# Performance work log

Hardware: AMD Instinct MI355X
Metric: run time of the kernel (lower is better)

Reference implementation:

```python
import jax, jax.numpy as jnp
import numpy as np

N_SEG = 64        # number of graphs in batch
NEG_SLOPE = 0.2   # PyG GATConv leaky_relu slope


def seg_softmax(vals, seg, num_segments):
    # vals: [E, H]; softmax over entries sharing the same segment id
    m = jax.ops.segment_max(vals, seg, num_segments=num_segments)
    m = jnp.where(jnp.isfinite(m), m, 0.0)  # guard empty segments
    e = jnp.exp(vals - m[seg])
    s = jax.ops.segment_sum(e, seg, num_segments=num_segments)
    return e / (s[seg] + 1e-16)


def setup_inputs() -> dict:
    key = jax.random.key(0)
    ks = jax.random.split(key, 16)
    N, E, Fin, H, C1, C2 = 50000, 800000, 128, 4, 32, 128
    x = jax.random.normal(ks[0], (N, Fin), jnp.float32)
    edge_index = jax.random.randint(ks[1], (2, E), 0, N)
    batch = jnp.sort(jax.random.randint(ks[2], (N,), 0, N_SEG))
    sc = lambda fan: 1.0 / np.sqrt(fan)
    W_gat = jax.random.normal(ks[3], (Fin, H * C1), jnp.float32) * sc(Fin)
    att_src = jax.random.normal(ks[4], (H, C1), jnp.float32) * sc(C1)
    att_dst = jax.random.normal(ks[5], (H, C1), jnp.float32) * sc(C1)
    b_gat = jnp.zeros((H * C1,), jnp.float32)
    bn1_w = jax.random.uniform(ks[6], (H * C1,), jnp.float32, 0.5, 1.5)
    bn1_b = jax.random.normal(ks[7], (H * C1,), jnp.float32) * 0.1
    W_gcn = jax.random.normal(ks[8], (H * C1, C2), jnp.float32) * sc(H * C1)
    b_gcn = jnp.zeros((C2,), jnp.float32)
    bn2_w = jax.random.uniform(ks[9], (C2,), jnp.float32, 0.5, 1.5)
    bn2_b = jax.random.normal(ks[10], (C2,), jnp.float32) * 0.1
    W_gate = jax.random.normal(ks[11], (C2, 1), jnp.float32) * sc(C2)
    b_gate = jnp.zeros((1,), jnp.float32)
    W_fc = jax.random.normal(ks[12], (C2, 1), jnp.float32) * sc(C2)
    b_fc = jnp.zeros((1,), jnp.float32)
    return dict(x=x, edge_index=edge_index, batch=batch, W_gat=W_gat,
                att_src=att_src, att_dst=att_dst, b_gat=b_gat,
                bn1_w=bn1_w, bn1_b=bn1_b, W_gcn=W_gcn, b_gcn=b_gcn,
                bn2_w=bn2_w, bn2_b=bn2_b, W_gate=W_gate, b_gate=b_gate,
                W_fc=W_fc, b_fc=b_fc)


def reference(x, edge_index, batch, W_gat, att_src, att_dst, b_gat,
              bn1_w, bn1_b, W_gcn, b_gcn, bn2_w, bn2_b,
              W_gate, b_gate, W_fc, b_fc):
    N = x.shape[0]
    H, C1 = att_src.shape
    loops = jnp.arange(N)
    src = jnp.concatenate([edge_index[0], loops])  # message source j
    dst = jnp.concatenate([edge_index[1], loops])  # aggregation target i

    # ---- GATConv (heads=4, concat, add_self_loops) ----
    h = (x @ W_gat).reshape(N, H, C1)                       # [N,H,C1]
    a_src = jnp.einsum('nhc,hc->nh', h, att_src)
    a_dst = jnp.einsum('nhc,hc->nh', h, att_dst)
    e = jax.nn.leaky_relu(a_src[src] + a_dst[dst], NEG_SLOPE)  # [E',H]
    alpha = seg_softmax(e, dst, N)
    msg = h[src] * alpha[..., None]                          # [E',H,C1]
    out1 = jax.ops.segment_sum(msg, dst, num_segments=N).reshape(N, H * C1) + b_gat
    out1 = jax.nn.elu(out1)
    out1 = out1 * bn1_w + bn1_b          # BatchNorm1d (eval: mean 0, var 1)
    # dropout: identity (eval mode)

    # ---- GCNConv (self-loops, symmetric normalization) ----
    deg = jax.ops.segment_sum(jnp.ones_like(dst, dtype=x.dtype), dst, num_segments=N)
    dinv = jax.lax.rsqrt(jnp.maximum(deg, 1.0))
    norm = dinv[src] * dinv[dst]                             # [E']
    h2 = out1 @ W_gcn                                        # [N,C2]
    out2 = jax.ops.segment_sum(h2[src] * norm[:, None], dst, num_segments=N) + b_gcn
    out2 = jax.nn.elu(out2)
    out2 = out2 * bn2_w + bn2_b

    # ---- GlobalAttention pooling ----
    gate = out2 @ W_gate + b_gate                            # [N,1]
    w = seg_softmax(gate, batch, N_SEG)
    graph_rep = jax.ops.segment_sum(w * out2, batch, num_segments=N_SEG)  # [G,C2]

    out = graph_rep @ W_fc + b_fc                            # [G,1]
    return out.squeeze(1)
```

## Files before the change

kernel.cpp:

```cpp
#include <hip/hip_runtime.h>
#include <math.h>


#define NEG_SLOPE 0.2f
#define BKT_BITS 7
#define BKT_SIZE 128
#define CHUNK_A 4096

typedef __attribute__((ext_vector_type(8))) short short8v;
typedef __attribute__((ext_vector_type(4))) float floatx4;

__device__ __forceinline__ int lower_bound_i(const int* a, int n, int key) {
    int lo = 0, hi = n;
    while (lo < hi) {
        int mid = (lo + hi) >> 1;
        if (a[mid] < key) lo = mid + 1; else hi = mid;
    }
    return lo;
}

__device__ __forceinline__ unsigned pack_bf16(float lo, float hi) {
    unsigned ua = __float_as_uint(lo);
    unsigned ub = __float_as_uint(hi);
    ua = ua + 0x7fffu + ((ua >> 16) & 1u);
    ub = ub + 0x7fffu + ((ub >> 16) & 1u);
    return (ua >> 16) | (ub & 0xffff0000u);
}

__device__ __forceinline__ unsigned short bf16_1(float v) {
    unsigned u = __float_as_uint(v);
    u = u + 0x7fffu + ((u >> 16) & 1u);
    return (unsigned short)(u >> 16);
}

__global__ __launch_bounds__(1024) void k_prep(
    const float* __restrict__ W1, const float* __restrict__ atts,
    const float* __restrict__ attd, const float* __restrict__ W2,
    unsigned short* __restrict__ Wt1, unsigned short* __restrict__ Wt2)
{
    if (blockIdx.x == 0) {
        for (int idx = threadIdx.x; idx < 144 * 128; idx += 1024) {
            int j = idx >> 7, i = idx & 127;
            float v;
            if (j < 128) v = W1[i * 128 + j];
            else if (j < 132) {
                int h = j - 128; float s = 0.f;
                for (int c = 0; c < 32; c++) s += W1[i * 128 + h * 32 + c] * atts[h * 32 + c];
                v = s;
            } else if (j < 136) {
                int h = j - 132; float s = 0.f;
                for (int c = 0; c < 32; c++) s += W1[i * 128 + h * 32 + c] * attd[h * 32 + c];
                v = s;
            } else v = 0.f;
            Wt1[idx] = bf16_1(v);
        }
    } else {
        for (int idx = threadIdx.x; idx < 144 * 128; idx += 1024) {
            int j = idx >> 7, i = idx & 127;
            Wt2[idx] = bf16_1(j < 128 ? W2[i * 128 + j] : 0.f);
        }
    }
}

__global__ __launch_bounds__(256) void k_gemm_mfma(
    const float* __restrict__ A, const unsigned short* __restrict__ Wt,
    unsigned* __restrict__ Cb, int N, int mode,
    const float* __restrict__ pb, const float* __restrict__ pw,
    const float* __restrict__ pb2, const float* __restrict__ dinv,
    float* __restrict__ aS, float* __restrict__ aD)
{
    __shared__ unsigned short sA[64 * 136];
    __shared__ unsigned short sB[144 * 136];
    const int tid = threadIdx.x;
    const int n0 = blockIdx.x * 64;

    {
        const uint4* Wg = (const uint4*)Wt;
#pragma unroll
        for (int i = 0; i < 9; i++) {
            int q = tid + 256 * i;
            uint4 v = Wg[q];
            int j = q >> 4, seg = q & 15;
            *(uint4*)(sB + j * 136 + seg * 8) = v;
        }
    }
    {
#pragma unroll
        for (int i = 0; i < 8; i++) {
            int g = tid + 256 * i;
            int r = g >> 5, w4 = g & 31;
            int gn = n0 + r;
            unsigned p0 = 0, p1 = 0;
            if (gn < N) {
                float4 v = *(const float4*)(A + (size_t)gn * 128 + w4 * 4);
                if (mode) {
                    int k = w4 * 4;
                    float4 bv = *(const float4*)(pb + k);
                    float4 wv = *(const float4*)(pw + k);
                    float4 b2 = *(const float4*)(pb2 + k);
                    float t;
                    t = v.x + bv.x; t = (t > 0.f) ? t : expm1f(t); v.x = t * wv.x + b2.x;
                    t = v.y + bv.y; t = (t > 0.f) ? t : expm1f(t); v.y = t * wv.y + b2.y;
                    t = v.z + bv.z; t = (t > 0.f) ? t : expm1f(t); v.z = t * wv.z + b2.z;
                    t = v.w + bv.w; t = (t > 0.f) ? t : expm1f(t); v.w = t * wv.w + b2.w;
                }
                p0 = pack_bf16(v.x, v.y);
                p1 = pack_bf16(v.z, v.w);
            }
            uint2 pv = make_uint2(p0, p1);
            *(uint2*)(sA + r * 136 + w4 * 4) = pv;
        }
    }
    __syncthreads();

    const int wid = tid >> 6, lane = tid & 63;
    const int quad = lane >> 4, l16 = lane & 15;

    floatx4 acc[9];
#pragma unroll
    for (int ct = 0; ct < 9; ct++) acc[ct] = (floatx4){0.f, 0.f, 0.f, 0.f};

    const unsigned short* pa = sA + (wid * 16 + l16) * 136 + quad * 8;
    const unsigned short* pbt = sB + l16 * 136 + quad * 8;
#pragma unroll
    for (int ks = 0; ks < 4; ks++) {
        short8v a = *(const short8v*)(pa + ks * 32);
#pragma unroll
        for (int ct = 0; ct < 9; ct++) {
            short8v b = *(const short8v*)(pbt + ct * (16 * 136) + ks * 32);
            acc[ct] = __builtin_amdgcn_mfma_f32_16x16x32_bf16(a, b, acc[ct], 0, 0, 0);
        }
    }

#pragma unroll
    for (int r = 0; r < 4; r++) {
        int n = n0 + wid * 16 + quad * 4 + r;
        if (n >= N) continue;
        float s = mode ? dinv[n] : 1.f;
#pragma unroll
        for (int ct = 0; ct < 4; ct++) {
            Cb[(size_t)n * 64 + ct * 16 + l16] =
                pack_bf16(acc[ct][r] * s, acc[ct + 4][r] * s);
        }
        if (mode == 0) {
            float e = acc[8][r];
            if (l16 < 4) aS[(size_t)n * 4 + l16] = e;
            else if (l16 < 8) aD[(size_t)n * 4 + (l16 - 4)] = e;
        }
    }
}

__global__ __launch_bounds__(256) void k_bhist(const int* __restrict__ dst,
                                               int* __restrict__ bcount,
                                               int E, int NB)
{
    __shared__ int h[512];
    const int tid = threadIdx.x;
    for (int i = tid; i < NB; i += 256) h[i] = 0;
    __syncthreads();
    int base = blockIdx.x * 2048;
#pragma unroll
    for (int k = 0; k < 8; k++) {
        int e = base + k * 256 + tid;
        if (e < E) atomicAdd(&h[dst[e] >> BKT_BITS], 1);
    }
    __syncthreads();
    for (int i = tid; i < NB; i += 256) {
        int c = h[i];
        if (c) atomicAdd(&bcount[i], c);
    }
}

__global__ __launch_bounds__(512) void k_bscan(const int* __restrict__ bcount,
                                               int* __restrict__ bb,
                                               int* __restrict__ bcur, int NB)
{
    __shared__ int sc[512];
    const int tid = threadIdx.x;
    int own = (tid < NB) ? bcount[tid] : 0;
    sc[tid] = own;
    __syncthreads();
    for (int st = 1; st < 512; st <<= 1) {
        int v = 0;
        if (tid >= st) v = sc[tid - st];
        __syncthreads();
        if (tid >= st) sc[tid] += v;
        __syncthreads();
    }
    int excl = sc[tid] - own;
    if (tid < NB) { bb[tid] = excl; bcur[tid] = excl; }
    if (tid == 511) { bb[NB] = sc[511]; bcur[NB] = sc[511]; }
}

__global__ __launch_bounds__(256) void k_binA(const int* __restrict__ ei,
                                              int* __restrict__ bcur,
                                              int2* __restrict__ pairs,
                                              int E, int NB)
{
    __shared__ int h[512];
    __shared__ int base[512];
    const int tid = threadIdx.x;
    for (int i = tid; i < NB + 1; i += 256) h[i] = 0;
    __syncthreads();
    const int c0 = blockIdx.x * CHUNK_A;
    int s[16], d[16], b[16];
#pragma unroll
    for (int k = 0; k < 16; k++) {
        int e = c0 + k * 256 + tid;
        bool v = e < E;
        s[k] = v ? ei[e] : 0;
        d[k] = v ? ei[E + e] : 0;
        b[k] = v ? (d[k] >> BKT_BITS) : NB;
        atomicAdd(&h[b[k]], 1);
    }
    __syncthreads();
    for (int i = tid; i < NB + 1; i += 256) {
        int c = h[i];
        base[i] = c ? atomicAdd(&bcur[i], c) : 0;
        h[i] = 0;
    }
    __syncthreads();
#pragma unroll
    for (int k = 0; k < 16; k++) {
        int r = atomicAdd(&h[b[k]], 1);
        pairs[base[b[k]] + r] = make_int2(s[k], d[k]);
    }
}

__global__ __launch_bounds__(256) void k_binB(const int2* __restrict__ pairs,
                                              const int* __restrict__ bb,
                                              int* __restrict__ csr,
                                              int* __restrict__ offs,
                                              float* __restrict__ dinv,
                                              int N, int NB, int E)
{
    __shared__ int hist[BKT_SIZE], start[BKT_SIZE], cur[BKT_SIZE];
    __shared__ int sc[BKT_SIZE];
    const int tid = threadIdx.x;
    const int b = blockIdx.x;
    const int d0 = b << BKT_BITS;
    const int pbg = bb[b], peg = bb[b + 1];

    if (tid < BKT_SIZE) { hist[tid] = 0; cur[tid] = 0; }
    __syncthreads();
    for (int i = pbg + tid; i < peg; i += 256)
        atomicAdd(&hist[pairs[i].y - d0], 1);
    __syncthreads();
    int own = (tid < BKT_SIZE) ? hist[tid] : 0;
    if (tid < BKT_SIZE) sc[tid] = own;
    __syncthreads();
    for (int st = 1; st < BKT_SIZE; st <<= 1) {
        int v = 0;
        bool act = (tid < BKT_SIZE) && (tid >= st);
        if (act) v = sc[tid - st];
        __syncthreads();
        if (act) sc[tid] += v;
        __syncthreads();
    }
    if (tid < BKT_SIZE) {
        int abs0 = pbg + (sc[tid] - own);
        start[tid] = abs0;
        int d = d0 + tid;
        if (d < N) {
            offs[d] = abs0;
            dinv[d] = rsqrtf((float)(own + 1));
        }
    }
    if (tid == 0 && b == NB - 1) offs[N] = E;
    __syncthreads();
    for (int i = pbg + tid; i < peg; i += 256) {
        int2 p = pairs[i];
        int ld = p.y - d0;
        int r = atomicAdd(&cur[ld], 1);
        csr[start[ld] + r] = p.x;
    }
}

__global__ __launch_bounds__(256) void k_gat_aggr(
    const unsigned* __restrict__ hb, const float* __restrict__ aSg,
    const float* __restrict__ aDg, const int* __restrict__ offs,
    const int* __restrict__ csr, float* __restrict__ raw1, int N)
{
    __shared__ __align__(16) float s_u[4][64][4];
    __shared__ int s_s[4][64];

    const int wid = threadIdx.x >> 6;
    const int lane = threadIdx.x & 63;
    const int n = blockIdx.x * 4 + wid;
    if (n >= N) return;

    const int beg = offs[n];
    const int cnt = offs[n + 1] - beg + 1;
    const float4 ad = *(const float4*)(aDg + (size_t)n * 4);
    const int hA = lane >> 5;
    const float* pu = &s_u[wid][0][2 * hA];
    const int* ps = &s_s[wid][0];

    float t0 = 0.f, t1 = 0.f, t2 = 0.f, t3 = 0.f;
    float accLo = 0.f, accHi = 0.f;

    for (int base = 0; base < cnt; base += 64) {
        int idx = base + lane;
        bool valid = idx < cnt;
        int src = n;
        if (valid && idx > 0) src = csr[beg + idx - 1];
        float u0 = 0.f, u1 = 0.f, u2 = 0.f, u3 = 0.f;
        if (valid) {
            float4 as = *(const float4*)(aSg + (size_t)src * 4);
            float l0 = as.x + ad.x; l0 = (l0 > 0.f) ? l0 : NEG_SLOPE * l0;
            float l1 = as.y + ad.y; l1 = (l1 > 0.f) ? l1 : NEG_SLOPE * l1;
            float l2 = as.z + ad.z; l2 = (l2 > 0.f) ? l2 : NEG_SLOPE * l2;
            float l3 = as.w + ad.w; l3 = (l3 > 0.f) ? l3 : NEG_SLOPE * l3;
            u0 = __expf(l0); u1 = __expf(l1); u2 = __expf(l2); u3 = __expf(l3);
        }
        t0 += u0; t1 += u1; t2 += u2; t3 += u3;
        s_s[wid][lane] = src;
        *(float4*)&s_u[wid][lane][0] = make_float4(u0, u2, u1, u3);

        int cc = min(64, cnt - base);
        int j = 0;
        for (; j + 8 <= cc; j += 8) {
            int sj[8]; float2 uj[8]; unsigned vv[8];
#pragma unroll
            for (int k = 0; k < 8; k++) sj[k] = ps[j + k];
#pragma unroll
            for (int k = 0; k < 8; k++) uj[k] = *(const float2*)&pu[(j + k) * 4];
#pragma unroll
            for (int k = 0; k < 8; k++) vv[k] = hb[sj[k] * 64 + lane];
#pragma unroll
            for (int k = 0; k < 8; k++) {
                float lo = __uint_as_float(vv[k] << 16);
                float hi = __uint_as_float(vv[k] & 0xffff0000u);
                accLo += uj[k].x * lo;
                accHi += uj[k].y * hi;
            }
        }
        for (; j < cc; j++) {
            int sj = ps[j];
            float2 uv = *(const float2*)&pu[j * 4];
            unsigned v = hb[sj * 64 + lane];
            accLo += uv.x * __uint_as_float(v << 16);
            accHi += uv.y * __uint_as_float(v & 0xffff0000u);
        }
    }
#pragma unroll
    for (int msk = 1; msk < 64; msk <<= 1) {
        t0 += __shfl_xor(t0, msk);
        t1 += __shfl_xor(t1, msk);
        t2 += __shfl_xor(t2, msk);
        t3 += __shfl_xor(t3, msk);
    }
    float sLo = (hA ? t1 : t0) + 1e-16f;
    float sHi = (hA ? t3 : t2) + 1e-16f;
    raw1[(size_t)n * 128 + lane]      = accLo / sLo;
    raw1[(size_t)n * 128 + 64 + lane] = accHi / sHi;
}

__global__ __launch_bounds__(256) void k_gcn_aggr(
    const unsigned* __restrict__ h2b, const int* __restrict__ offs,
    const int* __restrict__ csr, const float* __restrict__ dinv,
    const float* __restrict__ bgcn,
    const float* __restrict__ bn2w, const float* __restrict__ bn2b,
    const float* __restrict__ wgate, const float* __restrict__ bgate,
    const float* __restrict__ wfc,
    float* __restrict__ gate, float* __restrict__ fcdot, int N)
{
    __shared__ int s_s[4][64];

    const int wid = threadIdx.x >> 6;
    const int lane = threadIdx.x & 63;
    const int n = blockIdx.x * 4 + wid;
    if (n >= N) return;

    const int beg = offs[n];
    const int cnt = offs[n + 1] - beg + 1;
    const float dn = dinv[n];
    const int* ps = &s_s[wid][0];

    float accLo = 0.f, accHi = 0.f;
    for (int base = 0; base < cnt; base += 64) {
        int idx = base + lane;
        int src = n;
        if (idx > 0 && idx < cnt) src = csr[beg + idx - 1];
        s_s[wid][lane] = src;

        int cc = min(64, cnt - base);
        int j = 0;
        for (; j + 8 <= cc; j += 8) {
            int sj[8]; unsigned vv[8];
#pragma unroll
            for (int k = 0; k < 8; k++) sj[k] = ps[j + k];
#pragma unroll
            for (int k = 0; k < 8; k++) vv[k] = h2b[sj[k] * 64 + lane];
#pragma unroll
            for (int k = 0; k < 8; k++) {
                accLo += __uint_as_float(vv[k] << 16);
                accHi += __uint_as_float(vv[k] & 0xffff0000u);
            }
        }
        for (; j < cc; j++) {
            unsigned v = h2b[ps[j] * 64 + lane];
            accLo += __uint_as_float(v << 16);
            accHi += __uint_as_float(v & 0xffff0000u);
        }
    }
    float v0 = dn * accLo + bgcn[lane];
    v0 = (v0 > 0.f) ? v0 : expm1f(v0);
    v0 = v0 * bn2w[lane] + bn2b[lane];
    float v1 = dn * accHi + bgcn[lane + 64];
    v1 = (v1 > 0.f) ? v1 : expm1f(v1);
    v1 = v1 * bn2w[lane + 64] + bn2b[lane + 64];

    float g = v0 * wgate[lane] + v1 * wgate[lane + 64];
    float f = v0 * wfc[lane]   + v1 * wfc[lane + 64];
#pragma unroll
    for (int msk = 1; msk < 64; msk <<= 1) {
        g += __shfl_xor(g, msk);
        f += __shfl_xor(f, msk);
    }
    if (lane == 0) { gate[n] = g + bgate[0]; fcdot[n] = f; }
}

__global__ __launch_bounds__(256) void k_pool(
    const float* __restrict__ gate, const float* __restrict__ fcdot,
    const int* __restrict__ batch, const float* __restrict__ bfc,
    float* __restrict__ out, int N)
{
    __shared__ float red[256];
    __shared__ int range[2];
    const int g = blockIdx.x;
    const int tid = threadIdx.x;
    if (tid < 2) range[tid] = lower_bound_i(batch, N, g + tid);
    __syncthreads();
    const int lo = range[0], hi = range[1];
    float se = 0.f, sf = 0.f;
    for (int i = lo + tid; i < hi; i += 256) {
        float e = __expf(gate[i]);
        se += e;
        sf += e * fcdot[i];
    }
    red[tid] = se; __syncthreads();
    for (int s = 128; s > 0; s >>= 1) {
        if (tid < s) red[tid] += red[tid + s];
        __syncthreads();
    }
    se = red[0]; __syncthreads();
    red[tid] = sf; __syncthreads();
    for (int s = 128; s > 0; s >>= 1) {
        if (tid < s) red[tid] += red[tid + s];
        __syncthreads();
    }
    sf = red[0];
    if (tid == 0) out[g] = sf / (se + 1e-16f) + bfc[0];
}

extern "C" void kernel_launch(void* const* d_in, const int* in_sizes, int n_in,
                              void* d_out, int out_size, void* d_ws, size_t ws_size,
                              hipStream_t stream) {
    const float* x     = (const float*)d_in[0];
    const int*   ei    = (const int*)d_in[1];
    const int*   batch = (const int*)d_in[2];
    const float* Wgat  = (const float*)d_in[3];
    const float* atts  = (const float*)d_in[4];
    const float* attd  = (const float*)d_in[5];
    const float* bgat  = (const float*)d_in[6];
    const float* bn1w  = (const float*)d_in[7];
    const float* bn1b  = (const float*)d_in[8];
    const float* Wgcn  = (const float*)d_in[9];
    const float* bgcn  = (const float*)d_in[10];
    const float* bn2w  = (const float*)d_in[11];
    const float* bn2b  = (const float*)d_in[12];
    const float* wgate = (const float*)d_in[13];
    const float* bgate = (const float*)d_in[14];
    const float* wfc   = (const float*)d_in[15];
    const float* bfc   = (const float*)d_in[16];
    float* out = (float*)d_out;

    const int N = in_sizes[0] / 128;
    const int E = in_sizes[1] / 2;
    const int NB = (N + BKT_SIZE - 1) / BKT_SIZE;

    unsigned* hb  = (unsigned*)d_ws;
    unsigned* h2b = hb + (size_t)N * 64;
    float* raw1  = (float*)(h2b + (size_t)N * 64);
    int2* pairs  = (int2*)raw1;
    float* aS    = raw1 + (size_t)N * 128;
    float* aD    = aS + (size_t)N * 4;
    float* gate  = aD + (size_t)N * 4;
    float* fcdot = gate + N;
    float* dinv  = fcdot + N;
    int* offs   = (int*)(dinv + N);
    int* csr    = offs + (N + 1);
    int* bcount = csr + E;
    int* bb     = bcount + (NB + 1);
    int* bcur   = bb + (NB + 1);
    unsigned short* Wt1 = (unsigned short*)(bcur + (NB + 1));
    unsigned short* Wt2 = Wt1 + 144 * 128;

    hipMemsetAsync(bcount, 0, (size_t)(NB + 1) * sizeof(int), stream);

    const int gemm_blocks = (N + 63) / 64;
    const int aggr_blocks = (N + 3) / 4;

    k_prep<<<2, 1024, 0, stream>>>(Wgat, atts, attd, Wgcn, Wt1, Wt2);
    k_bhist<<<(E + 2047) / 2048, 256, 0, stream>>>(ei + E, bcount, E, NB);
    k_gemm_mfma<<<gemm_blocks, 256, 0, stream>>>(x, Wt1, hb, N, 0,
                                                 nullptr, nullptr, nullptr,
                                                 nullptr, aS, aD);
    k_bscan<<<1, 512, 0, stream>>>(bcount, bb, bcur, NB);
    k_binA<<<(E + CHUNK_A - 1) / CHUNK_A, 256, 0, stream>>>(ei, bcur, pairs, E, NB);
    k_binB<<<NB, 256, 0, stream>>>(pairs, bb, csr, offs, dinv, N, NB, E);
    k_gat_aggr<<<aggr_blocks, 256, 0, stream>>>(hb, aS, aD, offs, csr, raw1, N);
    k_gemm_mfma<<<gemm_blocks, 256, 0, stream>>>(raw1, Wt2, h2b, N, 1,
                                                 bgat, bn1w, bn1b, dinv,
                                                 nullptr, nullptr);
    k_gcn_aggr<<<aggr_blocks, 256, 0, stream>>>(h2b, offs, csr, dinv, bgcn,
                                                bn2w, bn2b, wgate, bgate, wfc,
                                                gate, fcdot, N);
    k_pool<<<64, 256, 0, stream>>>(gate, fcdot, batch, bfc, out, N);
}
```

Before: 276.7 us.

## Fuse weight prep with edge histogram, store GAT output as bf16, enlarge GEMM tiles

Merges the weight-preparation and destination-bucket histogram kernels into one launch. Each histogram block now writes a private slice, and the scan sums the slices, which removes the global atomics and the memset. The GAT aggregation output is written as bf16 instead of fp32, halving the traffic for the intermediate read by the second GEMM. The MFMA GEMM is templated on mode, processes 128 rows per block with two row tiles per wave, and skips the unused ninth column tile in mode 1. The trade-offs are an extra bf16 rounding before ELU/BN and heavier per-slice summation work in the single-block scan.

New measurement: 311.0 us. 12.4% more time.

```diff
diff --git a/kernel.cpp b/kernel.cpp
--- a/kernel.cpp
+++ b/kernel.cpp
@@ -33,16 +33,21 @@
     return (unsigned short)(u >> 16);
 }
 
-__global__ __launch_bounds__(1024) void k_prep(
+__global__ __launch_bounds__(256) void k_front(
     const float* __restrict__ W1, const float* __restrict__ atts,
     const float* __restrict__ attd, const float* __restrict__ W2,
-    unsigned short* __restrict__ Wt1, unsigned short* __restrict__ Wt2)
-{
-    if (blockIdx.x == 0) {
-        for (int idx = threadIdx.x; idx < 144 * 128; idx += 1024) {
+    unsigned short* __restrict__ Wt1, unsigned short* __restrict__ Wt2,
+    const int* __restrict__ dst, int* __restrict__ bhists, int E)
+{
+    const int b = blockIdx.x;
+    if (b < 2) {
+        const float* W = b ? W2 : W1;
+        unsigned short* Wt = b ? Wt2 : Wt1;
+        const int lim = b ? (128 * 128) : (144 * 128);
+        for (int idx = threadIdx.x; idx < lim; idx += 256) {
             int j = idx >> 7, i = idx & 127;
             float v;
-            if (j < 128) v = W1[i * 128 + j];
+            if (j < 128) v = W[i * 128 + j];
             else if (j < 132) {
                 int h = j - 128; float s = 0.f;
                 for (int c = 0; c < 32; c++) s += W1[i * 128 + h * 32 + c] * atts[h * 32 + c];
@@ -52,63 +57,97 @@
                 for (int c = 0; c < 32; c++) s += W1[i * 128 + h * 32 + c] * attd[h * 32 + c];
                 v = s;
             } else v = 0.f;
-            Wt1[idx] = bf16_1(v);
+            Wt[idx] = bf16_1(v);
         }
     } else {
-        for (int idx = threadIdx.x; idx < 144 * 128; idx += 1024) {
-            int j = idx >> 7, i = idx & 127;
-            Wt2[idx] = bf16_1(j < 128 ? W2[i * 128 + j] : 0.f);
-        }
-    }
-}
-
+        __shared__ int h[512];
+        const int tid = threadIdx.x;
+        for (int i = tid; i < 512; i += 256) h[i] = 0;
+        __syncthreads();
+        int base = (b - 2) * 2048;
+#pragma unroll
+        for (int k = 0; k < 8; k++) {
+            int e = base + k * 256 + tid;
+            if (e < E) atomicAdd(&h[dst[e] >> BKT_BITS], 1);
+        }
+        __syncthreads();
+        int* slice = bhists + (size_t)(b - 2) * 512;
+        for (int i = tid; i < 512; i += 256) slice[i] = h[i];
+    }
+}
+
+template<int MODE>
 __global__ __launch_bounds__(256) void k_gemm_mfma(
-    const float* __restrict__ A, const unsigned short* __restrict__ Wt,
-    unsigned* __restrict__ Cb, int N, int mode,
+    const void* __restrict__ Ain, const unsigned short* __restrict__ Wt,
+    unsigned* __restrict__ Cb, int N,
     const float* __restrict__ pb, const float* __restrict__ pw,
     const float* __restrict__ pb2, const float* __restrict__ dinv,
     float* __restrict__ aS, float* __restrict__ aD)
 {
-    __shared__ unsigned short sA[64 * 136];
-    __shared__ unsigned short sB[144 * 136];
+    constexpr int NCT = (MODE == 0) ? 9 : 8;
+    __shared__ unsigned short sA[128 * 136];
+    __shared__ unsigned short sB[NCT * 16 * 136];
     const int tid = threadIdx.x;
-    const int n0 = blockIdx.x * 64;
+    const int n0 = blockIdx.x * 128;
 
     {
         const uint4* Wg = (const uint4*)Wt;
-#pragma unroll
-        for (int i = 0; i < 9; i++) {
-            int q = tid + 256 * i;
+        const int nq = NCT * 16 * 16;
+        for (int q = tid; q < nq; q += 256) {
             uint4 v = Wg[q];
             int j = q >> 4, seg = q & 15;
             *(uint4*)(sB + j * 136 + seg * 8) = v;
         }
     }
-    {
-#pragma unroll
-        for (int i = 0; i < 8; i++) {
-            int g = tid + 256 * i;
-            int r = g >> 5, w4 = g & 31;
+    if (MODE == 0) {
+        const float* A = (const float*)Ain;
+        const int w4 = tid & 31;
+        const int r0 = tid >> 5;
+#pragma unroll
+        for (int i = 0; i < 16; i++) {
+            int r = r0 + 8 * i;
             int gn = n0 + r;
             unsigned p0 = 0, p1 = 0;
             if (gn < N) {
                 float4 v = *(const float4*)(A + (size_t)gn * 128 + w4 * 4);
-                if (mode) {
-                    int k = w4 * 4;
-                    float4 bv = *(const float4*)(pb + k);
-                    float4 wv = *(const float4*)(pw + k);
-                    float4 b2 = *(const float4*)(pb2 + k);
-                    float t;
-                    t = v.x + bv.x; t = (t > 0.f) ? t : expm1f(t); v.x = t * wv.x + b2.x;
-                    t = v.y + bv.y; t = (t > 0.f) ? t : expm1f(t); v.y = t * wv.y + b2.y;
-                    t = v.z + bv.z; t = (t > 0.f) ? t : expm1f(t); v.z = t * wv.z + b2.z;
-                    t = v.w + bv.w; t = (t > 0.f) ? t : expm1f(t); v.w = t * wv.w + b2.w;
-                }
                 p0 = pack_bf16(v.x, v.y);
                 p1 = pack_bf16(v.z, v.w);
             }
-            uint2 pv = make_uint2(p0, p1);
-            *(uint2*)(sA + r * 136 + w4 * 4) = pv;
+            *(uint2*)(sA + r * 136 + w4 * 4) = make_uint2(p0, p1);
+        }
+    } else {
+        const unsigned short* A = (const unsigned short*)Ain;
+        const int w8 = tid & 15;
+        const int r0 = tid >> 4;
+        const int k0 = w8 * 8;
+        float pbv[8], pwv[8], p2v[8];
+        *(float4*)(pbv)     = *(const float4*)(pb + k0);
+        *(float4*)(pbv + 4) = *(const float4*)(pb + k0 + 4);
+        *(float4*)(pwv)     = *(const float4*)(pw + k0);
+        *(float4*)(pwv + 4) = *(const float4*)(pw + k0 + 4);
+        *(float4*)(p2v)     = *(const float4*)(pb2 + k0);
+        *(float4*)(p2v + 4) = *(const float4*)(pb2 + k0 + 4);
+#pragma unroll
+        for (int i = 0; i < 8; i++) {
+            int r = r0 + 16 * i;
+            int gn = n0 + r;
+            uint4 outv = make_uint4(0, 0, 0, 0);
+            if (gn < N) {
+                uint4 v = *(const uint4*)(A + (size_t)gn * 128 + k0);
+                unsigned uu[4] = {v.x, v.y, v.z, v.w};
+                unsigned ro[4];
+#pragma unroll
+                for (int q2 = 0; q2 < 4; q2++) {
+                    float lo = __uint_as_float(uu[q2] << 16);
+                    float hi = __uint_as_float(uu[q2] & 0xffff0000u);
+                    float t;
+                    t = lo + pbv[2 * q2];     t = (t > 0.f) ? t : expm1f(t); lo = t * pwv[2 * q2]     + p2v[2 * q2];
+                    t = hi + pbv[2 * q2 + 1]; t = (t > 0.f) ? t : expm1f(t); hi = t * pwv[2 * q2 + 1] + p2v[2 * q2 + 1];
+                    ro[q2] = pack_bf16(lo, hi);
+                }
+                outv = make_uint4(ro[0], ro[1], ro[2], ro[3]);
+            }
+            *(uint4*)(sA + r * 136 + k0) = outv;
         }
     }
     __syncthreads();
@@ -116,68 +155,56 @@
     const int wid = tid >> 6, lane = tid & 63;
     const int quad = lane >> 4, l16 = lane & 15;
 
-    floatx4 acc[9];
-#pragma unroll
-    for (int ct = 0; ct < 9; ct++) acc[ct] = (floatx4){0.f, 0.f, 0.f, 0.f};
-
-    const unsigned short* pa = sA + (wid * 16 + l16) * 136 + quad * 8;
+    floatx4 acc[2][NCT];
+#pragma unroll
+    for (int rt = 0; rt < 2; rt++)
+#pragma unroll
+        for (int ct = 0; ct < NCT; ct++) acc[rt][ct] = (floatx4){0.f, 0.f, 0.f, 0.f};
+
+    const unsigned short* pa0 = sA + (wid * 32 + l16) * 136 + quad * 8;
     const unsigned short* pbt = sB + l16 * 136 + quad * 8;
 #pragma unroll
     for (int ks = 0; ks < 4; ks++) {
-        short8v a = *(const short8v*)(pa + ks * 32);
-#pragma unroll
-        for (int ct = 0; ct < 9; ct++) {
-            short8v b = *(const short8v*)(pbt + ct * (16 * 136) + ks * 32);
-            acc[ct] = __builtin_amdgcn_mfma_f32_16x16x32_bf16(a, b, acc[ct], 0, 0, 0);
-        }
-    }
-
-#pragma unroll
-    for (int r = 0; r < 4; r++) {
-        int n = n0 + wid * 16 + quad * 4 + r;
-        if (n >= N) continue;
-        float s = mode ? dinv[n] : 1.f;
-#pragma unroll
-        for (int ct = 0; ct < 4; ct++) {
-            Cb[(size_t)n * 64 + ct * 16 + l16] =
-                pack_bf16(acc[ct][r] * s, acc[ct + 4][r] * s);
-        }
-        if (mode == 0) {
-            float e = acc[8][r];
-            if (l16 < 4) aS[(size_t)n * 4 + l16] = e;
-            else if (l16 < 8) aD[(size_t)n * 4 + (l16 - 4)] = e;
-        }
-    }
-}
-
-__global__ __launch_bounds__(256) void k_bhist(const int* __restrict__ dst,
-                                               int* __restrict__ bcount,
-                                               int E, int NB)
-{
-    __shared__ int h[512];
-    const int tid = threadIdx.x;
-    for (int i = tid; i < NB; i += 256) h[i] = 0;
-    __syncthreads();
-    int base = blockIdx.x * 2048;
-#pragma unroll
-    for (int k = 0; k < 8; k++) {
-        int e = base + k * 256 + tid;
-        if (e < E) atomicAdd(&h[dst[e] >> BKT_BITS], 1);
-    }
-    __syncthreads();
-    for (int i = tid; i < NB; i += 256) {
-        int c = h[i];
-        if (c) atomicAdd(&bcount[i], c);
-    }
-}
-
-__global__ __launch_bounds__(512) void k_bscan(const int* __restrict__ bcount,
+        short8v a0 = *(const short8v*)(pa0 + ks * 32);
+        short8v a1 = *(const short8v*)(pa0 + 16 * 136 + ks * 32);
+#pragma unroll
+        for (int ct = 0; ct < NCT; ct++) {
+            short8v bv = *(const short8v*)(pbt + ct * (16 * 136) + ks * 32);
+            acc[0][ct] = __builtin_amdgcn_mfma_f32_16x16x32_bf16(a0, bv, acc[0][ct], 0, 0, 0);
+            acc[1][ct] = __builtin_amdgcn_mfma_f32_16x16x32_bf16(a1, bv, acc[1][ct], 0, 0, 0);
+        }
+    }
+
+#pragma unroll
+    for (int rt = 0; rt < 2; rt++) {
+#pragma unroll
+        for (int r = 0; r < 4; r++) {
+            int n = n0 + wid * 32 + rt * 16 + quad * 4 + r;
+            if (n >= N) continue;
+            float s = MODE ? dinv[n] : 1.f;
+#pragma unroll
+            for (int ct = 0; ct < 4; ct++) {
+                Cb[(size_t)n * 64 + ct * 16 + l16] =
+                    pack_bf16(acc[rt][ct][r] * s, acc[rt][ct + 4][r] * s);
+            }
+            if (MODE == 0) {
+                float e = acc[rt][8][r];
+                if (l16 < 4) aS[(size_t)n * 4 + l16] = e;
+                else if (l16 < 8) aD[(size_t)n * 4 + (l16 - 4)] = e;
+            }
+        }
+    }
+}
+
+__global__ __launch_bounds__(512) void k_bscan(const int* __restrict__ bhists,
+                                               int nslices,
                                                int* __restrict__ bb,
                                                int* __restrict__ bcur, int NB)
 {
     __shared__ int sc[512];
     const int tid = threadIdx.x;
-    int own = (tid < NB) ? bcount[tid] : 0;
+    int own = 0;
+    for (int s = 0; s < nslices; s++) own += bhists[(size_t)s * 512 + tid];
     sc[tid] = own;
     __syncthreads();
     for (int st = 1; st < 512; st <<= 1) {
@@ -279,7 +306,7 @@
 __global__ __launch_bounds__(256) void k_gat_aggr(
     const unsigned* __restrict__ hb, const float* __restrict__ aSg,
     const float* __restrict__ aDg, const int* __restrict__ offs,
-    const int* __restrict__ csr, float* __restrict__ raw1, int N)
+    const int* __restrict__ csr, unsigned short* __restrict__ raw1b, int N)
 {
     __shared__ __align__(16) float s_u[4][64][4];
     __shared__ int s_s[4][64];
@@ -352,8 +379,8 @@
     }
     float sLo = (hA ? t1 : t0) + 1e-16f;
     float sHi = (hA ? t3 : t2) + 1e-16f;
-    raw1[(size_t)n * 128 + lane]      = accLo / sLo;
-    raw1[(size_t)n * 128 + 64 + lane] = accHi / sHi;
+    raw1b[(size_t)n * 128 + lane]      = bf16_1(accLo / sLo);
+    raw1b[(size_t)n * 128 + 64 + lane] = bf16_1(accHi / sHi);
 }
 
 __global__ __launch_bounds__(256) void k_gcn_aggr(
@@ -479,41 +506,40 @@
     const int N = in_sizes[0] / 128;
     const int E = in_sizes[1] / 2;
     const int NB = (N + BKT_SIZE - 1) / BKT_SIZE;
+    const int NHB = (E + 2047) / 2048;
 
     unsigned* hb  = (unsigned*)d_ws;
     unsigned* h2b = hb + (size_t)N * 64;
-    float* raw1  = (float*)(h2b + (size_t)N * 64);
-    int2* pairs  = (int2*)raw1;
-    float* aS    = raw1 + (size_t)N * 128;
+    unsigned short* raw1b = (unsigned short*)(h2b + (size_t)N * 64);
+    int2* pairs  = (int2*)raw1b;
+    float* aS    = (float*)(raw1b + (size_t)N * 128);
     float* aD    = aS + (size_t)N * 4;
     float* gate  = aD + (size_t)N * 4;
     float* fcdot = gate + N;
     float* dinv  = fcdot + N;
     int* offs   = (int*)(dinv + N);
     int* csr    = offs + (N + 1);
-    int* bcount = csr + E;
-    int* bb     = bcount + (NB + 1);
+    int* bb     = csr + E;
     int* bcur   = bb + (NB + 1);
-    unsigned short* Wt1 = (unsigned short*)(bcur + (NB + 1));
+    int* bhists = bcur + (NB + 1);
+    unsigned short* Wt1 = (unsigned short*)(bhists + (size_t)NHB * 512);
     unsigned short* Wt2 = Wt1 + 144 * 128;
 
-    hipMemsetAsync(bcount, 0, (size_t)(NB + 1) * sizeof(int), stream);
-
-    const int gemm_blocks = (N + 63) / 64;
+    const int gemm_blocks = (N + 127) / 128;
     const int aggr_blocks = (N + 3) / 4;
 
-    k_prep<<<2, 1024, 0, stream>>>(Wgat, atts, attd, Wgcn, Wt1, Wt2);
-    k_bhist<<<(E + 2047) / 2048, 256, 0, stream>>>(ei + E, bcount, E, NB);
-    k_gemm_mfma<<<gemm_blocks, 256, 0, stream>>>(x, Wt1, hb, N, 0,
-                                                 nullptr, nullptr, nullptr,
-                                                 nullptr, aS, aD);
-    k_bscan<<<1, 512, 0, stream>>>(bcount, bb, bcur, NB);
+    k_front<<<NHB + 2, 256, 0, stream>>>(Wgat, atts, attd, Wgcn, Wt1, Wt2,
+                                         ei + E, bhists, E);
+    k_gemm_mfma<0><<<gemm_blocks, 256, 0, stream>>>(x, Wt1, hb, N,
+                                                    nullptr, nullptr, nullptr,
+                                                    nullptr, aS, aD);
+    k_bscan<<<1, 512, 0, stream>>>(bhists, NHB, bb, bcur, NB);
     k_binA<<<(E + CHUNK_A - 1) / CHUNK_A, 256, 0, stream>>>(ei, bcur, pairs, E, NB);
     k_binB<<<NB, 256, 0, stream>>>(pairs, bb, csr, offs, dinv, N, NB, E);
-    k_gat_aggr<<<aggr_blocks, 256, 0, stream>>>(hb, aS, aD, offs, csr, raw1, N);
-    k_gemm_mfma<<<gemm_blocks, 256, 0, stream>>>(raw1, Wt2, h2b, N, 1,
-                                                 bgat, bn1w, bn1b, dinv,
-                                                 nullptr, nullptr);
+    k_gat_aggr<<<aggr_blocks, 256, 0, stream>>>(hb, aS, aD, offs, csr, raw1b, N);
+    k_gemm_mfma<1><<<gemm_blocks, 256, 0, stream>>>(raw1b, Wt2, h2b, N,
+                                                    bgat, bn1w, bn1b, dinv,
+                                                    nullptr, nullptr);
     k_gcn_aggr<<<aggr_blocks, 256, 0, stream>>>(h2b, offs, csr, dinv, bgcn,
                                                 bn2w, bn2b, wgate, bgate, wfc,
                                                 gate, fcdot, N);
```
